# Optimization experiments

Hardware: AMD Instinct MI355X
Metric: run time of the kernel (lower is better)

## Reference

```python
import jax, jax.numpy as jnp
import numpy as np

B, C_IN, H, W = 8, 256, 32, 32
DK = 256
DV = 256
NH = 8
DKH = DK // NH  # 32
C_OUT = 512
KS, PAD = 3, 1


def setup_inputs() -> dict:
    key = jax.random.key(0)
    ks = jax.random.split(key, 9)
    s = 0.05
    return {
        "x": jax.random.normal(ks[0], (B, C_IN, H, W), jnp.float32),
        "w_qkv": jax.random.normal(ks[1], (2 * DK + DV, C_IN, 1, 1), jnp.float32) * s,
        "b_qkv": jnp.zeros((2 * DK + DV,), jnp.float32),
        "w_attn": jax.random.normal(ks[2], (DV, DV, 1, 1), jnp.float32) * s,
        "b_attn": jnp.zeros((DV,), jnp.float32),
        "w_out": jax.random.normal(ks[3], (C_OUT - DV, C_IN, KS, KS), jnp.float32) * s,
        "b_out": jnp.zeros((C_OUT - DV,), jnp.float32),
        # torch init: dkh**-0.5 + rand
        "key_rel_w": DKH ** (-0.5) + jax.random.uniform(ks[4], (2 * W - 1, DKH), jnp.float32),
        "key_rel_h": DKH ** (-0.5) + jax.random.uniform(ks[5], (2 * H - 1, DKH), jnp.float32),
    }


def conv2d(x, w, b, pad):
    y = jax.lax.conv_general_dilated(
        x, w, window_strides=(1, 1), padding=[(pad, pad), (pad, pad)],
        dimension_numbers=("NCHW", "OIHW", "NCHW"))
    return y + b[None, :, None, None]


def rel_to_abs(x):
    # x: [b, nh, L, 2L-1] -> [b, nh, L, L] (skew trick)
    b, nh, L, _ = x.shape
    x = jnp.pad(x, ((0, 0), (0, 0), (0, 0), (0, 1)))
    flat = x.reshape(b, nh, L * 2 * L)
    flat = jnp.pad(flat, ((0, 0), (0, 0), (0, L - 1)))
    final = flat.reshape(b, nh, L + 1, 2 * L - 1)
    return final[:, :, :L, L - 1:]


def relative_logits_1d(q, rel_k, Hd, Wd, transpose_mask):
    # q: [B, NH, DKH, Hd, Wd]; rel_k: [2*Wd-1, DKH]
    rel = jnp.einsum("bhdxy,md->bhxym", q, rel_k)          # [B,NH,Hd,Wd,2Wd-1]
    rel = rel.reshape(-1, NH * Hd, Wd, 2 * Wd - 1)
    rel = rel_to_abs(rel)                                   # [B,NH*Hd,Wd,Wd]
    rel = rel.reshape(-1, NH, Hd, 1, Wd, Wd)
    rel = jnp.broadcast_to(rel, (rel.shape[0], NH, Hd, Hd, Wd, Wd))
    rel = jnp.transpose(rel, transpose_mask)
    return rel.reshape(-1, NH, Hd * Wd, Hd * Wd)


def reference(x, w_qkv, b_qkv, w_attn, b_attn, w_out, b_out, key_rel_w, key_rel_h):
    conv_out = conv2d(x, w_out, b_out, PAD)                 # [B, C_OUT-DV, H, W]
    qkv = conv2d(x, w_qkv, b_qkv, 0)                        # [B, 2DK+DV, H, W]
    q, k, v = jnp.split(qkv, [DK, 2 * DK], axis=1)
    q = q.reshape(B, NH, DKH, H * W) * (DKH ** -0.5)        # scaled BEFORE rel logits (as in torch)
    k = k.reshape(B, NH, DKH, H * W)
    v = v.reshape(B, NH, DV // NH, H * W)
    logits = jnp.einsum("bhdl,bhdm->bhlm", q, k)            # [B,NH,HW,HW]
    q5 = q.reshape(B, NH, DKH, H, W)
    w_rel = relative_logits_1d(q5, key_rel_w, H, W, (0, 1, 2, 4, 3, 5))
    h_rel = relative_logits_1d(jnp.transpose(q5, (0, 1, 2, 4, 3)), key_rel_h, W, H, (0, 1, 4, 2, 5, 3))
    logits = logits + h_rel + w_rel
    weights = jax.nn.softmax(logits, axis=-1)
    attn = jnp.einsum("bhlm,bhdm->bhdl", weights, v)        # [B,NH,DVH,HW]
    attn = attn.reshape(B, DV, H, W)
    attn = conv2d(attn, w_attn, b_attn, 0)
    return jnp.concatenate([conv_out, attn], axis=1)        # [B, C_OUT, H, W]
```

## Files before the change

kernel.cpp:

```cpp
#include <hip/hip_runtime.h>
#include <hip/hip_bf16.h>


typedef __hip_bfloat16 bf16;
typedef __attribute__((ext_vector_type(8))) short bf16x8;
typedef __attribute__((ext_vector_type(4))) float f32x4;

__device__ __forceinline__ float bf2f(bf16 v) { return __bfloat162float(v); }
__device__ __forceinline__ float blo(unsigned int v) { return __uint_as_float(v << 16); }
__device__ __forceinline__ float bhi(unsigned int v) { return __uint_as_float(v & 0xffff0000u); }
__device__ __forceinline__ unsigned short f2bfbits(float f) {
  union { bf16 h; unsigned short u; } cv; cv.h = __float2bfloat16(f); return cv.u;
}
__device__ __forceinline__ short f2bfr(float f) {
  return (short)((__float_as_uint(f) + 0x8000u) >> 16);
}

__global__ __launch_bounds__(256) void prep_kernel(
    const float* __restrict__ x, const float* __restrict__ wout,
    bf16* __restrict__ xT, bf16* __restrict__ wob0, bf16* __restrict__ wob1)
{
  int bid = blockIdx.x, tid = threadIdx.x;
  if (bid < 2048) {
    __shared__ float t[32 * 33];
    int b = bid >> 8, rem = bid & 255;
    int ci0 = (rem >> 5) * 32, l0 = (rem & 31) * 32;
    {
      int ciL = tid >> 3, lL4 = (tid & 7) * 4;
      float4 v = *(const float4*)(x + (size_t)(b * 256 + ci0 + ciL) * 1024 + l0 + lL4);
      t[ciL * 33 + lL4 + 0] = v.x; t[ciL * 33 + lL4 + 1] = v.y;
      t[ciL * 33 + lL4 + 2] = v.z; t[ciL * 33 + lL4 + 3] = v.w;
    }
    __syncthreads();
    {
      int lL = tid >> 3, cS = (tid & 7) * 4;
      unsigned int p0 = (unsigned int)f2bfbits(t[(cS + 0) * 33 + lL]) |
                        ((unsigned int)f2bfbits(t[(cS + 1) * 33 + lL]) << 16);
      unsigned int p1 = (unsigned int)f2bfbits(t[(cS + 2) * 33 + lL]) |
                        ((unsigned int)f2bfbits(t[(cS + 3) * 33 + lL]) << 16);
      uint2 u2; u2.x = p0; u2.y = p1;
      *(uint2*)(xT + ((size_t)(b * 1024) + l0 + lL) * 256 + ci0 + cS) = u2;
    }
  } else {
    int t0 = (bid - 2048) * 256 + tid;
#pragma unroll
    for (int s = 0; s < 8; ++s) {
      int u = s * 9216 + t0;
      int chunkblk = u / 2304;
      int within = u - chunkblk * 2304;
      int co63 = within / 36;
      int r = within - co63 * 36;
      int kidx = r >> 2, cig = r & 3;
      int co = (chunkblk >> 3) * 64 + co63;
      int ci = (chunkblk & 7) * 32 + cig * 8;
      union { unsigned short h[8]; uint4 u4; } pk;
#pragma unroll
      for (int j = 0; j < 8; ++j)
        pk.h[j] = f2bfbits(wout[(size_t)(co * 256 + ci + j) * 9 + kidx]);
      bf16* dst = (chunkblk < 28) ? (wob0 + (size_t)chunkblk * 18432)
                                  : (wob1 + (size_t)(chunkblk - 28) * 18432);
      *(uint4*)(dst + (size_t)within * 8) = pk.u4;
    }
  }
}

__global__ __launch_bounds__(256) void convqkv_kernel(
    const bf16* __restrict__ xT,
    const bf16* __restrict__ wob0, const bf16* __restrict__ wob1,
    const float* __restrict__ b_out, float* __restrict__ out,
    const float* __restrict__ wq, const float* __restrict__ b_qkv,
    bf16* __restrict__ qT, bf16* __restrict__ kR, bf16* __restrict__ vW)
{
  __shared__ __align__(16) short smem[27104];
  int tid = threadIdx.x, lane = tid & 63, wave = tid >> 6;
  int m16 = lane & 15, quad = lane >> 4;

  if (blockIdx.x < 256) {
    short* wS = smem;
    short* xS = smem + 18944;
    int bid = blockIdx.x;
    int rc = bid & 7, cotile = (bid >> 3) & 3, b = bid >> 5;
    int y0 = rc * 4;

    f32x4 acc[8];
#pragma unroll
    for (int t = 0; t < 8; ++t) acc[t] = (f32x4){0.f, 0.f, 0.f, 0.f};

    for (int ck = 0; ck < 8; ++ck) {
      __syncthreads();
      int cb = cotile * 8 + ck;
      const bf16* wbase = (cb < 28) ? (wob0 + (size_t)cb * 18432)
                                    : (wob1 + (size_t)(cb - 28) * 18432);
#pragma unroll
      for (int r = 0; r < 9; ++r) {
        int u = r * 256 + tid;
        *(uint4*)(wS + (u / 36) * 296 + (u % 36) * 8) = *(const uint4*)(wbase + (size_t)u * 8);
      }
#pragma unroll
      for (int r = 0; r < 3; ++r) {
        int u = r * 256 + tid;
        int pos = u >> 2, seg = u & 3;
        int row = pos >> 5, col = pos & 31;
        int gy = y0 - 1 + row;
        uint4 val = make_uint4(0u, 0u, 0u, 0u);
        if (gy >= 0 && gy < 32)
          val = *(const uint4*)(xT + ((size_t)(b * 1024) + gy * 32 + col) * 256 + ck * 32 + seg * 8);
        *(uint4*)(xS + (row * 34 + col + 1) * 40 + seg * 8) = val;
      }
      if (tid < 48) {
        int pos = tid >> 2, seg = tid & 3;
        int row = pos >> 1, side = pos & 1;
        *(uint4*)(xS + (row * 34 + side * 33) * 40 + seg * 8) = make_uint4(0u, 0u, 0u, 0u);
      }
      __syncthreads();
#pragma unroll
      for (int kidx = 0; kidx < 9; ++kidx) {
        int dy = kidx / 3, dx = kidx - dy * 3;
        bf16x8 af = *(const bf16x8*)(wS + (wave * 16 + m16) * 296 + kidx * 32 + quad * 8);
#pragma unroll
        for (int t = 0; t < 8; ++t) {
          int row = (t >> 1) + dy;
          int col = (t & 1) * 16 + m16 + dx;
          bf16x8 bf = *(const bf16x8*)(xS + (row * 34 + col) * 40 + quad * 8);
          acc[t] = __builtin_amdgcn_mfma_f32_16x16x32_bf16(af, bf, acc[t], 0, 0, 0);
        }
      }
    }

    int cob = cotile * 64 + wave * 16 + quad * 4;
#pragma unroll
    for (int i = 0; i < 4; ++i) {
      float bv = b_out[cob + i];
#pragma unroll
      for (int t = 0; t < 8; ++t) {
        int y = y0 + (t >> 1), xc = (t & 1) * 16 + m16;
        out[((size_t)(b * 512) + cob + i) * 1024 + y * 32 + xc] = acc[t][i] + bv;
      }
    }
  } else {
    short* aS = smem;
    short* bS = smem + 4608;
    int bid2 = blockIdx.x - 256;
    int ltile = bid2 & 7;
    int rest = bid2 >> 3;
    int ctile = rest % 12;
    int b = rest / 12;
    int l0 = ltile * 128;
    int cbase = ctile * 64;

    f32x4 acc[8];
#pragma unroll
    for (int t = 0; t < 8; ++t) acc[t] = (f32x4){0.f, 0.f, 0.f, 0.f};

    for (int ck = 0; ck < 4; ++ck) {
      __syncthreads();
#pragma unroll
      for (int r = 0; r < 4; ++r) {
        int u = r * 256 + tid;
        int c = u >> 4, s4 = u & 15;
        float4 v = *(const float4*)(wq + (size_t)(cbase + c) * 256 + ck * 64 + s4 * 4);
        unsigned int p0 = (unsigned int)f2bfbits(v.x) | ((unsigned int)f2bfbits(v.y) << 16);
        unsigned int p1 = (unsigned int)f2bfbits(v.z) | ((unsigned int)f2bfbits(v.w) << 16);
        uint2 u2; u2.x = p0; u2.y = p1;
        *(uint2*)(aS + c * 72 + s4 * 4) = u2;
      }
#pragma unroll
      for (int r = 0; r < 4; ++r) {
        int u = r * 256 + tid;
        int l = u >> 3, seg = u & 7;
        *(uint4*)(bS + l * 72 + seg * 8) =
            *(const uint4*)(xT + ((size_t)(b * 1024) + l0 + l) * 256 + ck * 64 + seg * 8);
      }
      __syncthreads();
#pragma unroll
      for (int ks = 0; ks < 2; ++ks) {
        bf16x8 af = *(const bf16x8*)(aS + (wave * 16 + m16) * 72 + ks * 32 + quad * 8);
#pragma unroll
        for (int t = 0; t < 8; ++t) {
          bf16x8 bf = *(const bf16x8*)(bS + (t * 16 + m16) * 72 + ks * 32 + quad * 8);
          acc[t] = __builtin_amdgcn_mfma_f32_16x16x32_bf16(af, bf, acc[t], 0, 0, 0);
        }
      }
    }

    __syncthreads();
    short* ldsT = smem + wave * 3072;
    int cb = cbase + wave * 16;
    bool isq = (ctile < 4);
    float bv[4];
#pragma unroll
    for (int i = 0; i < 4; ++i) bv[i] = b_qkv[cb + quad * 4 + i];
#pragma unroll
    for (int t = 0; t < 8; ++t) {
#pragma unroll
      for (int i = 0; i < 4; ++i) {
        float v = acc[t][i] + bv[i];
        if (isq) v *= 0.17677669529663689f;
        ldsT[(t * 16 + m16) * 24 + quad * 4 + i] = (short)f2bfbits(v);
      }
    }
    if (ctile < 8) {
      bf16* dst = isq ? qT : kR;
      int coff = isq ? cb : cb - 256;
#pragma unroll
      for (int rep = 0; rep < 4; ++rep) {
        int u = rep * 64 + lane;
        int l = u >> 1, half = u & 1;
        int c0 = coff + half * 8;
        int head = b * 8 + (c0 >> 5), d0 = c0 & 31;
        *(uint4*)(dst + ((size_t)head * 1024 + l0 + l) * 32 + d0) =
            *(const uint4*)(ldsT + l * 24 + half * 8);
      }
    } else {
      int dcol = lane >> 2, lg = lane & 3;
      int c2 = (cb - 512) + dcol;
      int head = b * 8 + (c2 >> 5), gd = c2 & 31;
#pragma unroll
      for (int s = 0; s < 4; ++s) {
        union { unsigned int w[4]; uint4 u4; } pk;
#pragma unroll
        for (int p = 0; p < 4; ++p) {
          int j0 = lg * 32 + s * 8 + p * 2;
          unsigned int u0 = (unsigned short)ldsT[j0 * 24 + dcol];
          unsigned int u1 = (unsigned short)ldsT[(j0 + 1) * 24 + dcol];
          pk.w[p] = u0 | (u1 << 16);
        }
        *(uint4*)(vW + ((size_t)head * 32 + gd) * 1024 + l0 + lg * 32 + s * 8) = pk.u4;
      }
    }
  }
}

__global__ __launch_bounds__(256) void attn_mfma_kernel(
    const bf16* __restrict__ qT, const bf16* __restrict__ kR, const bf16* __restrict__ vW,
    const float* __restrict__ krw, const float* __restrict__ krh,
    bf16* __restrict__ attL)
{
  __shared__ __align__(16) char smem[31232];
  short* kaugS  = (short*)smem;
  short* vtS    = (short*)(smem + 13312);
  short* atileS = (short*)(smem + 17920);
  float* krwS   = (float*)smem;
  float* krhS   = krwS + 63 * 33;

  int tid = threadIdx.x;
  int lane = tid & 63, wave = tid >> 6;
  int m16 = lane & 15, quad = lane >> 4;
  int bid = blockIdx.x;
  int head = ((bid & 7) << 3) | ((bid >> 3) & 7);
  int qt = bid >> 6;
  int row0 = qt * 64;
  int b = head >> 3, h = head & 7;

  int skey = tid >> 2, sseg = tid & 3;
  int svd = tid >> 3, svk = tid & 7;
  const bf16* kptr = kR + (size_t)head * 32768 + skey * 32 + sseg * 8;
  const bf16* vptr = vW + (size_t)head * 32768 + svd * 1024 + svk * 8;
  uint4 kreg = *(const uint4*)kptr;
  uint4 vreg = *(const uint4*)vptr;

  for (int i = tid; i < 504; i += 256) {
    int row = i >> 3, d0 = (i & 7) * 4;
    float4 a = *(const float4*)(krw + row * 32 + d0);
    krwS[row * 33 + d0 + 0] = a.x; krwS[row * 33 + d0 + 1] = a.y;
    krwS[row * 33 + d0 + 2] = a.z; krwS[row * 33 + d0 + 3] = a.w;
    float4 c = *(const float4*)(krh + row * 32 + d0);
    krhS[row * 33 + d0 + 0] = c.x; krhS[row * 33 + d0 + 1] = c.y;
    krhS[row * 33 + d0 + 2] = c.z; krhS[row * 33 + d0 + 3] = c.w;
  }
  {
    int r = tid >> 2, seg = tid & 3;
    uint4 u = *(const uint4*)(qT + ((size_t)head * 1024 + row0 + r) * 32 + seg * 8);
    *(uint4*)(atileS + r * 104 + seg * 8) = u;
  }
  __syncthreads();

  {
    int r = tid >> 2, jseg = tid & 3;
    int qi = r & 31;
    int qx = qt * 2 + (r >> 5);
    float q32[32];
#pragma unroll
    for (int s4 = 0; s4 < 4; ++s4) {
      uint4 u = ((const uint4*)(atileS + r * 104))[s4];
      q32[s4 * 8 + 0] = blo(u.x); q32[s4 * 8 + 1] = bhi(u.x);
      q32[s4 * 8 + 2] = blo(u.y); q32[s4 * 8 + 3] = bhi(u.y);
      q32[s4 * 8 + 4] = blo(u.z); q32[s4 * 8 + 5] = bhi(u.z);
      q32[s4 * 8 + 6] = blo(u.w); q32[s4 * 8 + 7] = bhi(u.w);
    }
    unsigned int pw[4], ph[4];
#pragma unroll
    for (int jp = 0; jp < 4; ++jp) {
      float sv[4] = {0.f, 0.f, 0.f, 0.f};
#pragma unroll 2
      for (int half = 0; half < 2; ++half) {
        int j = jseg * 8 + jp * 2 + half;
        const float* kw = krwS + (j - qi + 31) * 33;
        const float* kh = krhS + (j - qx + 31) * 33;
        float s1 = 0.f, s2 = 0.f;
#pragma unroll
        for (int d = 0; d < 32; ++d) { s1 += q32[d] * kw[d]; s2 += q32[d] * kh[d]; }
        sv[half] = s1; sv[2 + half] = s2;
      }
      pw[jp] = (unsigned int)(unsigned short)f2bfr(sv[0]) |
               ((unsigned int)(unsigned short)f2bfr(sv[1]) << 16);
      ph[jp] = (unsigned int)(unsigned short)f2bfr(sv[2]) |
               ((unsigned int)(unsigned short)f2bfr(sv[3]) << 16);
    }
#pragma unroll
    for (int jp = 0; jp < 4; ++jp) {
      ((unsigned int*)(atileS + r * 104 + 32 + jseg * 8))[jp] = pw[jp];
      ((unsigned int*)(atileS + r * 104 + 64 + jseg * 8))[jp] = ph[jp];
    }
  }
  __syncthreads();

  {
    union { short s[16]; uint4 u4[2]; } oh;
#pragma unroll
    for (int e = 0; e < 16; ++e) oh.s[e] = 0;
    int base = 32 + sseg * 16;
    int pos = 32 + (skey & 31);
    if (pos >= base && pos < base + 16) oh.s[pos - base] = (short)0x3F80;
    ((uint4*)(kaugS + skey * 104 + 32 + sseg * 16))[0] = oh.u4[0];
    *((uint4*)(kaugS + skey * 104 + 32 + sseg * 16) + 1) = oh.u4[1];
  }

  bf16x8 afrag[3];
  {
    int arow = wave * 16 + m16;
#pragma unroll
    for (int ks = 0; ks < 3; ++ks)
      afrag[ks] = *(const bf16x8*)(atileS + arow * 104 + ks * 32 + quad * 8);
  }

  f32x4 oacc[2];
  oacc[0] = (f32x4){0.f, 0.f, 0.f, 0.f};
  oacc[1] = (f32x4){0.f, 0.f, 0.f, 0.f};
  float rsp[4] = {0.f, 0.f, 0.f, 0.f};
  short* pS = (short*)(smem + 17920) + wave * 1152;

  for (int c = 0; c < 16; ++c) {
    __syncthreads();
    *(uint4*)(kaugS + skey * 104 + sseg * 8) = kreg;
    if (sseg == 0) {
      if (c) kaugS[skey * 104 + 64 + (c - 1) * 2 + (skey >> 5)] = 0;
      kaugS[skey * 104 + 64 + c * 2 + (skey >> 5)] = (short)0x3F80;
    }
    *(uint4*)(vtS + svd * 72 + svk * 8) = vreg;
    if (c < 15) {
      kreg = *(const uint4*)(kptr + (c + 1) * 2048);
      vreg = *(const uint4*)(vptr + (c + 1) * 64);
    }
    __syncthreads();

    f32x4 sacc[4];
#pragma unroll
    for (int t = 0; t < 4; ++t) sacc[t] = (f32x4){0.f, 0.f, 0.f, 0.f};
#pragma unroll
    for (int t = 0; t < 4; ++t) {
#pragma unroll
      for (int ks = 0; ks < 3; ++ks) {
        bf16x8 bfK = *(const bf16x8*)(kaugS + (t * 16 + m16) * 104 + ks * 32 + quad * 8);
        sacc[t] = __builtin_amdgcn_mfma_f32_16x16x32_bf16(afrag[ks], bfK, sacc[t], 0, 0, 0);
      }
    }
#pragma unroll
    for (int t = 0; t < 4; ++t) {
#pragma unroll
      for (int i = 0; i < 4; ++i) {
        float e = __expf(sacc[t][i]);
        rsp[i] += e;
        pS[(quad * 4 + i) * 72 + t * 16 + m16] = f2bfr(e);
      }
    }
#pragma unroll
    for (int ks2 = 0; ks2 < 2; ++ks2) {
      bf16x8 pf = *(const bf16x8*)(pS + m16 * 72 + ks2 * 32 + quad * 8);
#pragma unroll
      for (int dt = 0; dt < 2; ++dt) {
        bf16x8 vf = *(const bf16x8*)(vtS + (dt * 16 + m16) * 72 + ks2 * 32 + quad * 8);
        oacc[dt] = __builtin_amdgcn_mfma_f32_16x16x32_bf16(pf, vf, oacc[dt], 0, 0, 0);
      }
    }
  }

#pragma unroll
  for (int off = 1; off < 16; off <<= 1)
#pragma unroll
    for (int i = 0; i < 4; ++i) rsp[i] += __shfl_xor(rsp[i], off, 64);
#pragma unroll
  for (int i = 0; i < 4; ++i) {
    float invs = 1.0f / rsp[i];
    int grow = row0 + wave * 16 + quad * 4 + i;
#pragma unroll
    for (int dt = 0; dt < 2; ++dt) {
      attL[((size_t)b * 1024 + grow) * 256 + h * 32 + dt * 16 + m16] =
          __float2bfloat16(oacc[dt][i] * invs);
    }
  }
}

__global__ __launch_bounds__(256) void attnout_mfma_kernel(
    const bf16* __restrict__ attL, const float* __restrict__ w, const float* __restrict__ bias,
    float* __restrict__ out)
{
  __shared__ __align__(16) short smem[13824];
  short* aS = smem;
  short* bS = smem + 4608;

  int tid = threadIdx.x, lane = tid & 63, wave = tid >> 6;
  int m16 = lane & 15, quad = lane >> 4;
  int l0 = blockIdx.x * 128;
  int cotile = blockIdx.y;
  int b = blockIdx.z;
  int cbase = cotile * 64;

  f32x4 acc[8];
#pragma unroll
  for (int t = 0; t < 8; ++t) acc[t] = (f32x4){0.f, 0.f, 0.f, 0.f};

  for (int ck = 0; ck < 4; ++ck) {
    __syncthreads();
#pragma unroll
    for (int r = 0; r < 4; ++r) {
      int u = r * 256 + tid;
      int c = u >> 4, s4 = u & 15;
      float4 v = *(const float4*)(w + (size_t)(cbase + c) * 256 + ck * 64 + s4 * 4);
      unsigned int p0 = (unsigned int)f2bfbits(v.x) | ((unsigned int)f2bfbits(v.y) << 16);
      unsigned int p1 = (unsigned int)f2bfbits(v.z) | ((unsigned int)f2bfbits(v.w) << 16);
      uint2 u2; u2.x = p0; u2.y = p1;
      *(uint2*)(aS + c * 72 + s4 * 4) = u2;
    }
#pragma unroll
    for (int r = 0; r < 4; ++r) {
      int u = r * 256 + tid;
      int l = u >> 3, seg = u & 7;
      *(uint4*)(bS + l * 72 + seg * 8) =
          *(const uint4*)(attL + ((size_t)(b * 1024) + l0 + l) * 256 + ck * 64 + seg * 8);
    }
    __syncthreads();
#pragma unroll
    for (int ks = 0; ks < 2; ++ks) {
      bf16x8 af = *(const bf16x8*)(aS + (wave * 16 + m16) * 72 + ks * 32 + quad * 8);
#pragma unroll
      for (int t = 0; t < 8; ++t) {
        bf16x8 bf = *(const bf16x8*)(bS + (t * 16 + m16) * 72 + ks * 32 + quad * 8);
        acc[t] = __builtin_amdgcn_mfma_f32_16x16x32_bf16(af, bf, acc[t], 0, 0, 0);
      }
    }
  }

  int co = cbase + wave * 16 + quad * 4;
#pragma unroll
  for (int i = 0; i < 4; ++i) {
    float bv = bias[co + i];
    size_t obase = ((size_t)(b * 512) + 256 + co + i) * 1024 + l0;
#pragma unroll
    for (int t = 0; t < 8; ++t)
      out[obase + t * 16 + m16] = acc[t][i] + bv;
  }
}

extern "C" void kernel_launch(void* const* d_in, const int* in_sizes, int n_in,
                              void* d_out, int out_size, void* d_ws, size_t ws_size,
                              hipStream_t stream) {
  const float* x      = (const float*)d_in[0];
  const float* w_qkv  = (const float*)d_in[1];
  const float* b_qkv  = (const float*)d_in[2];
  const float* w_attn = (const float*)d_in[3];
  const float* b_attn = (const float*)d_in[4];
  const float* w_out  = (const float*)d_in[5];
  const float* b_out  = (const float*)d_in[6];
  const float* krw    = (const float*)d_in[7];
  const float* krh    = (const float*)d_in[8];
  float* out = (float*)d_out;

  bf16* ws    = (bf16*)d_ws;
  bf16* xT    = ws;
  bf16* attL  = ws;
  bf16* qT    = ws + 2097152;
  bf16* kR    = ws + 4194304;
  bf16* vW    = ws + 6291456;

  bf16* wob0 = (bf16*)(out + (size_t)(0 * 512 + 256) * 1024);
  bf16* wob1 = (bf16*)(out + (size_t)(1 * 512 + 256) * 1024);

  prep_kernel<<<dim3(2084), 256, 0, stream>>>(x, w_out, xT, wob0, wob1);
  convqkv_kernel<<<dim3(1024), 256, 0, stream>>>(xT, wob0, wob1, b_out, out,
                                                 w_qkv, b_qkv, qT, kR, vW);
  attn_mfma_kernel<<<dim3(1024), 256, 0, stream>>>(qT, kR, vW, krw, krh, attL);
  attnout_mfma_kernel<<<dim3(8, 4, 8), 256, 0, stream>>>(attL, w_attn, b_attn, out);
}
```

Measured before the change: 163.2 us.

## Add relative logits in fp32 registers instead of augmenting K with one-hot MFMA

The relative-position logits were previously folded into the QK MFMA by widening A with bf16 rel-w/rel-h columns and K with one-hot indicator columns, costing three MFMAs per tile. Now the rel-w and rel-h terms are computed in fp32, stored in LDS, and added to the single-MFMA QK scores before the exponential. This also removes the bf16 rounding of the rel logits. The krw/krh tables are staged through one LDS buffer in sequence, which adds syncs, and each chunk iteration does extra LDS reads for the rel-h values.

New measurement: 151.8 us. -7.0%, faster.

```diff
diff --git a/kernel.cpp b/kernel.cpp
--- a/kernel.cpp
+++ b/kernel.cpp
@@ -236,12 +236,12 @@
     const float* __restrict__ krw, const float* __restrict__ krh,
     bf16* __restrict__ attL)
 {
-  __shared__ __align__(16) char smem[31232];
-  short* kaugS  = (short*)smem;
-  short* vtS    = (short*)(smem + 13312);
-  short* atileS = (short*)(smem + 17920);
-  float* krwS   = (float*)smem;
-  float* krhS   = krwS + 63 * 33;
+  __shared__ __align__(16) char smem[27648];
+  short* kS   = (short*)smem;
+  short* vtS  = (short*)(smem + 5120);
+  float* stgF = (float*)smem;
+  float* rhS  = (float*)(smem + 9728);
+  float* rwS  = (float*)(smem + 18432);
 
   int tid = threadIdx.x;
   int lane = tid & 63, wave = tid >> 6;
@@ -259,94 +259,91 @@
   uint4 kreg = *(const uint4*)kptr;
   uint4 vreg = *(const uint4*)vptr;
 
-  for (int i = tid; i < 504; i += 256) {
-    int row = i >> 3, d0 = (i & 7) * 4;
-    float4 a = *(const float4*)(krw + row * 32 + d0);
-    krwS[row * 33 + d0 + 0] = a.x; krwS[row * 33 + d0 + 1] = a.y;
-    krwS[row * 33 + d0 + 2] = a.z; krwS[row * 33 + d0 + 3] = a.w;
-    float4 c = *(const float4*)(krh + row * 32 + d0);
-    krhS[row * 33 + d0 + 0] = c.x; krhS[row * 33 + d0 + 1] = c.y;
-    krhS[row * 33 + d0 + 2] = c.z; krhS[row * 33 + d0 + 3] = c.w;
-  }
+  int r = tid >> 2, jseg = tid & 3;
+  float q32[32];
   {
-    int r = tid >> 2, seg = tid & 3;
-    uint4 u = *(const uint4*)(qT + ((size_t)head * 1024 + row0 + r) * 32 + seg * 8);
-    *(uint4*)(atileS + r * 104 + seg * 8) = u;
-  }
-  __syncthreads();
-
-  {
-    int r = tid >> 2, jseg = tid & 3;
-    int qi = r & 31;
-    int qx = qt * 2 + (r >> 5);
-    float q32[32];
+    const bf16* qp = qT + ((size_t)head * 1024 + row0 + r) * 32;
 #pragma unroll
     for (int s4 = 0; s4 < 4; ++s4) {
-      uint4 u = ((const uint4*)(atileS + r * 104))[s4];
+      uint4 u = ((const uint4*)qp)[s4];
       q32[s4 * 8 + 0] = blo(u.x); q32[s4 * 8 + 1] = bhi(u.x);
       q32[s4 * 8 + 2] = blo(u.y); q32[s4 * 8 + 3] = bhi(u.y);
       q32[s4 * 8 + 4] = blo(u.z); q32[s4 * 8 + 5] = bhi(u.z);
       q32[s4 * 8 + 6] = blo(u.w); q32[s4 * 8 + 7] = bhi(u.w);
     }
-    unsigned int pw[4], ph[4];
-#pragma unroll
-    for (int jp = 0; jp < 4; ++jp) {
-      float sv[4] = {0.f, 0.f, 0.f, 0.f};
-#pragma unroll 2
-      for (int half = 0; half < 2; ++half) {
-        int j = jseg * 8 + jp * 2 + half;
-        const float* kw = krwS + (j - qi + 31) * 33;
-        const float* kh = krhS + (j - qx + 31) * 33;
-        float s1 = 0.f, s2 = 0.f;
-#pragma unroll
-        for (int d = 0; d < 32; ++d) { s1 += q32[d] * kw[d]; s2 += q32[d] * kh[d]; }
-        sv[half] = s1; sv[2 + half] = s2;
-      }
-      pw[jp] = (unsigned int)(unsigned short)f2bfr(sv[0]) |
-               ((unsigned int)(unsigned short)f2bfr(sv[1]) << 16);
-      ph[jp] = (unsigned int)(unsigned short)f2bfr(sv[2]) |
-               ((unsigned int)(unsigned short)f2bfr(sv[3]) << 16);
-    }
-#pragma unroll
-    for (int jp = 0; jp < 4; ++jp) {
-      ((unsigned int*)(atileS + r * 104 + 32 + jseg * 8))[jp] = pw[jp];
-      ((unsigned int*)(atileS + r * 104 + 64 + jseg * 8))[jp] = ph[jp];
-    }
+  }
+
+  for (int i = tid; i < 504; i += 256) {
+    int row = i >> 3, d0 = (i & 7) * 4;
+    *(float4*)(stgF + row * 36 + d0) = *(const float4*)(krw + row * 32 + d0);
   }
   __syncthreads();
 
   {
-    union { short s[16]; uint4 u4[2]; } oh;
-#pragma unroll
-    for (int e = 0; e < 16; ++e) oh.s[e] = 0;
-    int base = 32 + sseg * 16;
-    int pos = 32 + (skey & 31);
-    if (pos >= base && pos < base + 16) oh.s[pos - base] = (short)0x3F80;
-    ((uint4*)(kaugS + skey * 104 + 32 + sseg * 16))[0] = oh.u4[0];
-    *((uint4*)(kaugS + skey * 104 + 32 + sseg * 16) + 1) = oh.u4[1];
-  }
-
-  bf16x8 afrag[3];
+    int qi = r & 31;
+#pragma unroll
+    for (int jj2 = 0; jj2 < 2; ++jj2) {
+      float rv[4];
+#pragma unroll
+      for (int jp = 0; jp < 4; ++jp) {
+        int j = jseg * 8 + jj2 * 4 + jp;
+        const float* kw = stgF + (j - qi + 31) * 36;
+        float s1 = 0.f;
+#pragma unroll
+        for (int d4 = 0; d4 < 8; ++d4) {
+          float4 kv = *(const float4*)(kw + d4 * 4);
+          s1 += q32[d4 * 4 + 0] * kv.x + q32[d4 * 4 + 1] * kv.y +
+                q32[d4 * 4 + 2] * kv.z + q32[d4 * 4 + 3] * kv.w;
+        }
+        rv[jp] = s1;
+      }
+      *(float4*)(rwS + r * 36 + jseg * 8 + jj2 * 4) = make_float4(rv[0], rv[1], rv[2], rv[3]);
+    }
+  }
+  __syncthreads();
+
+  for (int i = tid; i < 504; i += 256) {
+    int row = i >> 3, d0 = (i & 7) * 4;
+    *(float4*)(stgF + row * 36 + d0) = *(const float4*)(krh + row * 32 + d0);
+  }
+  __syncthreads();
+
   {
-    int arow = wave * 16 + m16;
-#pragma unroll
-    for (int ks = 0; ks < 3; ++ks)
-      afrag[ks] = *(const bf16x8*)(atileS + arow * 104 + ks * 32 + quad * 8);
-  }
+    int qx = qt * 2 + (r >> 5);
+#pragma unroll
+    for (int jj = 0; jj < 8; ++jj) {
+      int j = jseg * 8 + jj;
+      const float* kh = stgF + (j - qx + 31) * 36;
+      float s2 = 0.f;
+#pragma unroll
+      for (int d4 = 0; d4 < 8; ++d4) {
+        float4 kv = *(const float4*)(kh + d4 * 4);
+        s2 += q32[d4 * 4 + 0] * kv.x + q32[d4 * 4 + 1] * kv.y +
+              q32[d4 * 4 + 2] * kv.z + q32[d4 * 4 + 3] * kv.w;
+      }
+      rhS[j * 68 + r] = s2;
+    }
+  }
+  __syncthreads();
+
+  bf16x8 afrag = *(const bf16x8*)(
+      qT + ((size_t)head * 1024 + row0 + wave * 16 + m16) * 32 + quad * 8);
+  float rwreg[2][4];
+#pragma unroll
+  for (int par = 0; par < 2; ++par)
+#pragma unroll
+    for (int i = 0; i < 4; ++i)
+      rwreg[par][i] = rwS[(wave * 16 + quad * 4 + i) * 36 + par * 16 + m16];
 
   f32x4 oacc[2];
   oacc[0] = (f32x4){0.f, 0.f, 0.f, 0.f};
   oacc[1] = (f32x4){0.f, 0.f, 0.f, 0.f};
   float rsp[4] = {0.f, 0.f, 0.f, 0.f};
-  short* pS = (short*)(smem + 17920) + wave * 1152;
+  short* pS = (short*)(smem + 18432) + wave * 1152;
 
   for (int c = 0; c < 16; ++c) {
     __syncthreads();
-    *(uint4*)(kaugS + skey * 104 + sseg * 8) = kreg;
-    if (sseg == 0) {
-      if (c) kaugS[skey * 104 + 64 + (c - 1) * 2 + (skey >> 5)] = 0;
-      kaugS[skey * 104 + 64 + c * 2 + (skey >> 5)] = (short)0x3F80;
-    }
+    *(uint4*)(kS + skey * 40 + sseg * 8) = kreg;
     *(uint4*)(vtS + svd * 72 + svk * 8) = vreg;
     if (c < 15) {
       kreg = *(const uint4*)(kptr + (c + 1) * 2048);
@@ -354,22 +351,22 @@
     }
     __syncthreads();
 
+    float4 rh0 = *(const float4*)(rhS + (c * 2 + 0) * 68 + wave * 16 + quad * 4);
+    float4 rh1 = *(const float4*)(rhS + (c * 2 + 1) * 68 + wave * 16 + quad * 4);
+    float rhv[2][4] = {{rh0.x, rh0.y, rh0.z, rh0.w}, {rh1.x, rh1.y, rh1.z, rh1.w}};
+
     f32x4 sacc[4];
 #pragma unroll
-    for (int t = 0; t < 4; ++t) sacc[t] = (f32x4){0.f, 0.f, 0.f, 0.f};
-#pragma unroll
     for (int t = 0; t < 4; ++t) {
-#pragma unroll
-      for (int ks = 0; ks < 3; ++ks) {
-        bf16x8 bfK = *(const bf16x8*)(kaugS + (t * 16 + m16) * 104 + ks * 32 + quad * 8);
-        sacc[t] = __builtin_amdgcn_mfma_f32_16x16x32_bf16(afrag[ks], bfK, sacc[t], 0, 0, 0);
-      }
+      bf16x8 bfK = *(const bf16x8*)(kS + (t * 16 + m16) * 40 + quad * 8);
+      f32x4 z = (f32x4){0.f, 0.f, 0.f, 0.f};
+      sacc[t] = __builtin_amdgcn_mfma_f32_16x16x32_bf16(afrag, bfK, z, 0, 0, 0);
     }
 #pragma unroll
     for (int t = 0; t < 4; ++t) {
 #pragma unroll
       for (int i = 0; i < 4; ++i) {
-        float e = __expf(sacc[t][i]);
+        float e = __expf(sacc[t][i] + rwreg[t & 1][i] + rhv[t >> 1][i]);
         rsp[i] += e;
         pS[(quad * 4 + i) * 72 + t * 16 + m16] = f2bfr(e);
       }
```
